# Optimization experiments

Measured on AMD Instinct MI355X. Metric: run time of the kernel, lower is better.

The kernel has to match this reference:

```python
import jax, jax.numpy as jnp
import numpy as np

B, H, W = 8, 160, 180
PHASES = 3
DELTA = 0.01
GAMMA = 1.0


def _conv(a, k):
    return jax.lax.conv_general_dilated(a, k, (1, 1), 'SAME',
                                        dimension_numbers=('NCHW', 'OIHW', 'NCHW'))


def _cconv(xr, xi, kr, ki):
    # complex conv via 4 real convs: (xr+i xi) * (kr+i ki)
    return _conv(xr, kr) - _conv(xi, ki), _conv(xr, ki) + _conv(xi, kr)


def _t(k):
    # conv_transpose2d(stride=1, pad=1, 3x3) == conv2d with swapped in/out channels and spatially flipped kernel
    return jnp.flip(jnp.swapaxes(k, 0, 1), axis=(2, 3))


def _cconvT(xr, xi, kr, ki):
    return _cconv(xr, xi, _t(kr), _t(ki))


def _act(x):
    # eq. (33): smoothed ReLU; quadratic inside |x| <= delta
    return jnp.where(jnp.abs(x) > DELTA, jax.nn.relu(x),
                     x * x / (4 * DELTA) + 0.5 * x + DELTA / 4)


def _act_der(x):
    return jnp.where(jnp.abs(x) > DELTA, (x > 0).astype(x.dtype),
                     x / (2 * DELTA) + 0.5)


def _grad_r(xc, convs, thr):
    # gradient of smoothed L2-channel-norm regularizer (grad_r_x1 / grad_r_x2)
    xr = jnp.real(xc).reshape(-1, 1, H, W)
    xi = jnp.imag(xc).reshape(-1, 1, H, W)
    acts = []
    ar, ai = xr, xi
    for kr, ki in convs[:3]:
        pr, pi = _cconv(ar, ai, kr, ki)
        ar, ai = _act(pr), _act(pi)
        acts.append((ar, ai))
    w4r, w4i = _cconv(ar, ai, *convs[3])
    norm = jnp.sqrt(jnp.sum(w4r * w4r + w4i * w4i, axis=1, keepdims=True))
    I1 = (norm > thr).astype(w4r.dtype)
    denom = jnp.maximum(norm, 1e-12)  # F.normalize eps
    gr = I1 * (w4r / denom) + (1 - I1) * (w4r / thr)
    gi = I1 * (w4i / denom) + (1 - I1) * (w4i / thr)
    gr, gi = _cconvT(gr, gi, *convs[3])
    for j in (2, 1, 0):
        # NOTE: faithful to source — derivative evaluated at the ACTIVATED values, complex multiply
        dr, di = _act_der(acts[j][0]), _act_der(acts[j][1])
        gr, gi = gr * dr - gi * di, gr * di + gi * dr
        gr, gi = _cconvT(gr, gi, *convs[j])
    return (gr + 1j * gi).reshape(-1, H, W)


def _grad_f(xc, kc, mask):
    # F^H( M o (M o F x - k) ): mriAdjointOp(mriForwardOp(x,m) - k, m)
    return jnp.fft.ifft2((jnp.fft.fft2(xc) * mask - kc) * mask)


def _forward(x1, x2, k1, k2, mask, convsA, convsB, thr1, thr2, a1, a2, b1, b2):
    to_c = lambda a: a[:, 0] + 1j * a[:, 1]
    x1c, x2c, k1c, k2c = to_c(x1), to_c(x2), to_c(k1), to_c(k2)
    for i in range(PHASES):
        x1c = x1c - a1[i] * _grad_f(x1c, k1c, mask) - b1[i] * _grad_r(x1c, convsA, thr1[0] * GAMMA)
        x2c = x2c - a2[i] * _grad_f(x2c, k2c, mask) - b2[i] * _grad_r(x2c, convsB, thr2[0] * GAMMA)
    return jnp.stack([jnp.real(x1c), jnp.imag(x1c), jnp.real(x2c), jnp.imag(x2c)], axis=1)


def setup_inputs() -> dict:
    key = jax.random.key(0)
    ks = jax.random.split(key, 32)
    d = {}
    d['x1'] = jax.random.normal(ks[0], (B, 2, H, W), jnp.float32)
    d['x2'] = jax.random.normal(ks[1], (B, 2, H, W), jnp.float32)
    d['k1'] = jax.random.normal(ks[2], (B, 2, H, W), jnp.float32)
    d['k2'] = jax.random.normal(ks[3], (B, 2, H, W), jnp.float32)
    d['mask'] = jax.random.uniform(ks[4], (H, W), jnp.float32)
    conv_names = ['conv1r', 'conv1i', 'conv2r', 'conv2i', 'conv3r', 'conv3i', 'conv4r', 'conv4i',
                  'conv1r_', 'conv1i_', 'conv2r_', 'conv2i_', 'conv3r_', 'conv3i_', 'conv4r_', 'conv4i_']
    for j, name in enumerate(conv_names):
        cin = 1 if name.startswith('conv1') else 32
        d[name] = 0.06 * jax.random.normal(ks[5 + j], (32, cin, 3, 3), jnp.float32)  # ~xavier
    d['soft_thr1'] = jnp.full((1,), 0.01, jnp.float32)
    d['soft_thr2'] = jnp.full((1,), 0.01, jnp.float32)
    d['alphas1'] = jnp.full((PHASES,), 0.5, jnp.float32)
    d['alphas2'] = jnp.full((PHASES,), 0.5, jnp.float32)
    d['betas1'] = jnp.full((PHASES,), 0.1, jnp.float32)
    d['betas2'] = jnp.full((PHASES,), 0.1, jnp.float32)
    return d


def reference(x1, x2, k1, k2, mask,
              conv1r, conv1i, conv2r, conv2i, conv3r, conv3i, conv4r, conv4i,
              conv1r_, conv1i_, conv2r_, conv2i_, conv3r_, conv3i_, conv4r_, conv4i_,
              soft_thr1, soft_thr2, alphas1, alphas2, betas1, betas2):
    convsA = [(conv1r, conv1i), (conv2r, conv2i), (conv3r, conv3i), (conv4r, conv4i)]
    convsB = [(conv1r_, conv1i_), (conv2r_, conv2i_), (conv3r_, conv3i_), (conv4r_, conv4i_)]
    return _forward(x1, x2, k1, k2, mask, convsA, convsB,
                    soft_thr1, soft_thr2, alphas1, alphas2, betas1, betas2)
```

## Files before the change

kernel.cpp:

```cpp
#include <hip/hip_runtime.h>
#include <math.h>

#define HH 160
#define WW 180
#define HWSZ (HH*WW)
#define BB 8
#define BB2 16
#define P1 ((size_t)BB*HWSZ)
#define PE2 ((size_t)BB2*32*HWSZ)

typedef unsigned short u16;
typedef unsigned long long ull;
typedef __attribute__((ext_vector_type(8))) short short8;
typedef __attribute__((ext_vector_type(2))) unsigned long long ull2;
typedef __attribute__((ext_vector_type(4))) float floatx4;

struct Ptrs16 { const float* p[16]; };

__device__ __forceinline__ u16 f2b(float f) {
  unsigned u = __builtin_bit_cast(unsigned, f);
  unsigned r = (u + 0x7fffu + ((u >> 16) & 1u)) >> 16;
  return (u16)r;
}
__device__ __forceinline__ float b2f(u16 h) {
  return __builtin_bit_cast(float, ((unsigned)h) << 16);
}

__device__ __forceinline__ float actf(float x) {
  float q = x*x*25.0f + 0.5f*x + 0.0025f;
  float r = fmaxf(x, 0.0f);
  return (fabsf(x) > 0.01f) ? r : q;
}
__device__ __forceinline__ float actdf(float x) {
  float q = x*50.0f + 0.5f;
  float r = (x > 0.0f) ? 1.0f : 0.0f;
  return (fabsf(x) > 0.01f) ? r : q;
}

__global__ void prep_all(Ptrs16 ps, u16* __restrict__ dst0) {
  const int rIdx[12] = {2,4,6,6,4,2,10,12,14,14,12,10};
  const int bwdF[12] = {0,0,0,1,1,1,0,0,0,1,1,1};
  int slot = blockIdx.x / 36;
  int idx = (blockIdx.x % 36)*256 + threadIdx.x;
  if (idx >= 9*32*32) return;
  const float* wr = ps.p[rIdx[slot]];
  const float* wi = ps.p[rIdx[slot]+1];
  u16* dst = dst0 + (size_t)slot*18432;
  int tap = idx >> 10; int rem = idx & 1023; int o = rem >> 5; int c = rem & 31;
  int s = bwdF[slot] ? ((c*32 + o)*9 + (8 - tap)) : ((o*32 + c)*9 + tap);
  float vr = wr[s], vi = wi[s];
  int nt = o >> 4, m = o & 15;
  size_t base = (((size_t)tap*2 + nt)*2*16 + (size_t)m)*32 + c;
  dst[base]       = f2b(vr);
  dst[base + 512] = f2b(vi);
}

template<int MODE>
__global__ __launch_bounds__(256, 6)
void conv_mfma(const u16* __restrict__ inb, const u16* __restrict__ wbA,
               const u16* __restrict__ wbB, u16* __restrict__ outb,
               const u16* __restrict__ derb,
               const float* __restrict__ thrA, const float* __restrict__ thrB)
{
  __shared__ alignas(128) u16 stg[2*6*34*32];
  const int tid = threadIdx.x;
  const int lane = tid & 63, wv = tid >> 6;
  const int x0 = blockIdx.x * 32, y0 = blockIdx.y * 4, b = blockIdx.z;
  const u16* wb = (b < BB) ? wbA : wbB;
  const int m = lane & 15, q = lane >> 4;

  for (int j = tid; j < 1632; j += 256) {
    int prow = j / 136; int rem = j - prow*136;
    int col = rem >> 2, chq = rem & 3;
    int plane = prow / 6, row = prow - plane*6;
    int gy = y0 - 1 + row, gx = x0 - 1 + col;
    ull v0 = 0, v1 = 0;
    if (gy >= 0 && gy < HH && gx >= 0 && gx < WW) {
      const ull* src = (const ull*)(inb + (size_t)plane*PE2
                                    + (((size_t)b*HH + gy)*WW + gx)*32 + chq*8);
      v0 = src[0]; v1 = src[1];
    }
    int B = prow*2176 + col*64 + chq*16;
    B ^= ((B >> 7) & 7) << 4;
    ull* dst = (ull*)((char*)stg + B);
    dst[0] = v0; dst[1] = v1;
  }
  __syncthreads();

  floatx4 accr[2][2], acci[2][2];
#pragma unroll
  for (int s = 0; s < 2; ++s)
#pragma unroll
    for (int nt = 0; nt < 2; ++nt) {
      accr[s][nt] = (floatx4){0.f,0.f,0.f,0.f};
      acci[s][nt] = (floatx4){0.f,0.f,0.f,0.f};
    }

#pragma unroll
  for (int tap = 0; tap < 9; ++tap) {
    const int ky = tap / 3, kx = tap - ky*3;
    short8 Pr[2], Pi[2];
#pragma unroll
    for (int s = 0; s < 2; ++s) {
      int col = s*16 + m + kx;
      int BR = ((wv + ky)*34 + col)*64 + q*16;
      int BI = BR + 13056;
      BR ^= ((BR >> 7) & 7) << 4;
      BI ^= ((BI >> 7) & 7) << 4;
      const ull* pR = (const ull*)((const char*)stg + BR);
      const ull* pI = (const ull*)((const char*)stg + BI);
      ull2 vr; vr.x = pR[0]; vr.y = pR[1];
      ull2 vi; vi.x = pI[0]; vi.y = pI[1];
      Pr[s] = __builtin_bit_cast(short8, vr);
      Pi[s] = __builtin_bit_cast(short8, vi);
    }
#pragma unroll
    for (int nt = 0; nt < 2; ++nt) {
      const u16* pw = wb + (size_t)(tap*2 + nt)*1024 + (size_t)m*32 + q*8;
      short8 Wr = *(const short8*)pw;
      short8 Wi = *(const short8*)(pw + 512);
      ull2 wx = __builtin_bit_cast(ull2, Wi);
      wx.x ^= 0x8000800080008000ULL;
      wx.y ^= 0x8000800080008000ULL;
      short8 nWi = __builtin_bit_cast(short8, wx);
#pragma unroll
      for (int s = 0; s < 2; ++s) {
        accr[s][nt] = __builtin_amdgcn_mfma_f32_16x16x32_bf16(Wr,  Pr[s], accr[s][nt], 0, 0, 0);
        accr[s][nt] = __builtin_amdgcn_mfma_f32_16x16x32_bf16(nWi, Pi[s], accr[s][nt], 0, 0, 0);
        acci[s][nt] = __builtin_amdgcn_mfma_f32_16x16x32_bf16(Wr,  Pi[s], acci[s][nt], 0, 0, 0);
        acci[s][nt] = __builtin_amdgcn_mfma_f32_16x16x32_bf16(Wi,  Pr[s], acci[s][nt], 0, 0, 0);
      }
    }
  }

  const int y = y0 + wv;
#pragma unroll
  for (int s = 0; s < 2; ++s) {
    int x = x0 + s*16 + m;
    bool ok = (x < WW);
    float invn = 1.0f;
    if constexpr (MODE == 3) {
      float ss = 0.f;
#pragma unroll
      for (int nt = 0; nt < 2; ++nt)
#pragma unroll
        for (int r = 0; r < 4; ++r)
          ss += accr[s][nt][r]*accr[s][nt][r] + acci[s][nt][r]*acci[s][nt][r];
      ss += __shfl_xor(ss, 16, 64);
      ss += __shfl_xor(ss, 32, 64);
      float thr = (b < BB ? thrA : thrB)[0];
      invn = 1.0f / fmaxf(sqrtf(ss), thr);
    }
    size_t pxbase = (((size_t)b*HH + y)*WW + x)*32;
#pragma unroll
    for (int nt = 0; nt < 2; ++nt) {
      size_t gb = pxbase + nt*16 + q*4;
      ull dR = 0, dI = 0;
      if constexpr (MODE == 2) {
        if (ok) { dR = *(const ull*)(derb + gb); dI = *(const ull*)(derb + PE2 + gb); }
      }
      ull vR = 0, vI = 0;
#pragma unroll
      for (int r = 0; r < 4; ++r) {
        float pr = accr[s][nt][r], pi = acci[s][nt][r];
        if constexpr (MODE == 1) { pr = actf(pr); pi = actf(pi); }
        if constexpr (MODE == 3) { pr *= invn; pi *= invn; }
        if constexpr (MODE == 2) {
          float dr = actdf(b2f((u16)(dR >> (16*r))));
          float di = actdf(b2f((u16)(dI >> (16*r))));
          float nr = pr*dr - pi*di;
          pi = pr*di + pi*dr; pr = nr;
        }
        vR |= (ull)f2b(pr) << (16*r);
        vI |= (ull)f2b(pi) << (16*r);
      }
      if (ok) {
        *(ull*)(outb + gb)       = vR;
        *(ull*)(outb + PE2 + gb) = vI;
      }
    }
  }
}

__global__ __launch_bounds__(256)
void l1fwd(const float* __restrict__ xall,
           const float* __restrict__ wrA, const float* __restrict__ wiA,
           const float* __restrict__ wrB, const float* __restrict__ wiB,
           u16* __restrict__ outb)
{
  __shared__ float hR[10][12], hI[10][12];
  __shared__ float wt[9][32][2];
  const int tid = threadIdx.x;
  const int og = tid & 3, px = tid >> 2;
  const int lx = px & 7, ly = px >> 3;
  const int x0 = blockIdx.x*8, y0 = blockIdx.y*8, b = blockIdx.z;
  const int branch = b >> 3, img = b & 7;
  const float* wr = branch ? wrB : wrA;
  const float* wi = branch ? wiB : wiA;
  const float* xp = xall + (size_t)branch*2*P1 + (size_t)img*HWSZ;

  for (int j = tid; j < 576; j += 256) {
    int tap = j >> 6; int rem = j & 63; int o = rem >> 1, ri = rem & 1;
    wt[tap][o][ri] = ri ? wi[o*9+tap] : wr[o*9+tap];
  }
  for (int j = tid; j < 200; j += 256) {
    int plane = j / 100; int pos = j - plane*100;
    int yy = pos / 10, xx = pos - yy*10;
    int gy = y0 - 1 + yy, gx = x0 - 1 + xx;
    float v = 0.f;
    if (gy >= 0 && gy < HH && gx >= 0 && gx < WW)
      v = xp[(size_t)plane*P1 + (size_t)gy*WW + gx];
    (plane ? hI : hR)[yy][xx] = v;
  }
  __syncthreads();

  float accR[8], accI[8];
#pragma unroll
  for (int o = 0; o < 8; ++o) { accR[o] = 0.f; accI[o] = 0.f; }
#pragma unroll
  for (int tap = 0; tap < 9; ++tap) {
    int ky = tap/3, kx = tap - ky*3;
    float ar = hR[ly+ky][lx+kx], ai = hI[ly+ky][lx+kx];
#pragma unroll
    for (int o = 0; o < 8; ++o) {
      float wrv = wt[tap][og*8+o][0], wiv = wt[tap][og*8+o][1];
      accR[o] += ar*wrv - ai*wiv;
      accI[o] += ar*wiv + ai*wrv;
    }
  }
  int gx = x0 + lx, gy = y0 + ly;
  if (gx < WW) {
    size_t base = (((size_t)b*HH + gy)*WW + gx)*32 + og*8;
    ull* dR = (ull*)(outb + base);
    ull* dI = (ull*)(outb + PE2 + base);
#pragma unroll
    for (int k = 0; k < 2; ++k) {
      ull vR = 0, vI = 0;
#pragma unroll
      for (int t = 0; t < 4; ++t) {
        vR |= (ull)f2b(actf(accR[k*4+t])) << (16*t);
        vI |= (ull)f2b(actf(accI[k*4+t])) << (16*t);
      }
      dR[k] = vR; dI[k] = vI;
    }
  }
}

__global__ __launch_bounds__(256)
void l1bwd(const u16* __restrict__ gb,
           const float* __restrict__ wrA, const float* __restrict__ wiA,
           const float* __restrict__ wrB, const float* __restrict__ wiB,
           float* __restrict__ outp)
{
  __shared__ alignas(16) u16 stg[2*100*32];
  __shared__ float wt[32][9][2];
  const int tid = threadIdx.x;
  const int cg = tid & 3, px = tid >> 2;
  const int lx = px & 7, ly = px >> 3;
  const int x0 = blockIdx.x*8, y0 = blockIdx.y*8, b = blockIdx.z;
  const int branch = b >> 3, img = b & 7;
  const float* wr = branch ? wrB : wrA;
  const float* wi = branch ? wiB : wiA;

  for (int j = tid; j < 576; j += 256) {
    int c = j / 18; int rem = j - c*18; int tap = rem >> 1, ri = rem & 1;
    wt[c][tap][ri] = (ri ? wi : wr)[c*9 + (8-tap)];
  }
  for (int j = tid; j < 800; j += 256) {
    int plane = j / 400; int rem = j - plane*400;
    int pos = rem >> 2, chq = rem & 3;
    int yy = pos / 10, xx = pos - yy*10;
    int gy = y0 - 1 + yy, gx = x0 - 1 + xx;
    ull v0 = 0, v1 = 0;
    if (gy >= 0 && gy < HH && gx >= 0 && gx < WW) {
      const ull* src = (const ull*)(gb + (size_t)plane*PE2
                                    + (((size_t)b*HH + gy)*WW + gx)*32 + chq*8);
      v0 = src[0]; v1 = src[1];
    }
    ull* dst = (ull*)&stg[((size_t)plane*100 + pos)*32 + chq*8];
    dst[0] = v0; dst[1] = v1;
  }
  __syncthreads();

  float gr = 0.f, gi = 0.f;
#pragma unroll
  for (int tap = 0; tap < 9; ++tap) {
    int ky = tap/3, kx = tap - ky*3;
    int pos = (ly+ky)*10 + (lx+kx);
    const ull* pR = (const ull*)&stg[(size_t)pos*32 + cg*8];
    const ull* pI = (const ull*)&stg[(100 + (size_t)pos)*32 + cg*8];
    ull r0 = pR[0], r1 = pR[1], i0 = pI[0], i1 = pI[1];
#pragma unroll
    for (int t = 0; t < 4; ++t) {
      int c = cg*8 + t;
      float ar = b2f((u16)(r0 >> (16*t))), ai = b2f((u16)(i0 >> (16*t)));
      float wrv = wt[c][tap][0], wiv = wt[c][tap][1];
      gr += ar*wrv - ai*wiv;
      gi += ar*wiv + ai*wrv;
    }
#pragma unroll
    for (int t = 0; t < 4; ++t) {
      int c = cg*8 + 4 + t;
      float ar = b2f((u16)(r1 >> (16*t))), ai = b2f((u16)(i1 >> (16*t)));
      float wrv = wt[c][tap][0], wiv = wt[c][tap][1];
      gr += ar*wrv - ai*wiv;
      gi += ar*wiv + ai*wrv;
    }
  }
  gr += __shfl_xor(gr, 1, 64); gr += __shfl_xor(gr, 2, 64);
  gi += __shfl_xor(gi, 1, 64); gi += __shfl_xor(gi, 2, 64);

  int gx = x0 + lx, gy = y0 + ly;
  if (cg == 0 && gx < WW) {
    size_t o2 = (size_t)branch*2*P1 + (size_t)img*HWSZ + (size_t)gy*WW + gx;
    outp[o2]      = gr;
    outp[P1 + o2] = gi;
  }
}

__global__ void gen_dft2(float2* __restrict__ Mf, float2* __restrict__ Mi, int N) {
  int idx = blockIdx.x*256 + threadIdx.x;
  if (idx >= N*N) return;
  int r = idx / N, c = idx - r*N;
  long mm = ((long)r * (long)c) % N;
  double a = 2.0 * 3.14159265358979323846 * (double)mm / (double)N;
  double cs = cos(a), sn = sin(a);
  Mf[idx] = make_float2((float)cs, (float)(-sn));
  Mi[idx] = make_float2((float)(cs/N), (float)(sn/N));
}

__global__ void dft_row_planes(const float* __restrict__ xall,
                               float2* __restrict__ out, const float2* __restrict__ M) {
  int bh = blockIdx.x;
  int v = threadIdx.x; if (v >= WW) return;
  int b2 = bh / HH, h = bh - b2*HH;
  int branch = b2 >> 3, img = b2 & 7;
  const float* rowR = xall + (size_t)branch*2*P1 + (size_t)img*HWSZ + (size_t)h*WW;
  const float* rowI = rowR + P1;
  float ar = 0.f, ai = 0.f;
  for (int w = 0; w < WW; ++w) {
    float sr = rowR[w], si = rowI[w];
    float2 m = M[w*WW + v];
    ar += sr*m.x - si*m.y;
    ai += sr*m.y + si*m.x;
  }
  out[(size_t)bh*WW + v] = make_float2(ar, ai);
}

__global__ void dft_row_c(const float2* __restrict__ in, float2* __restrict__ out,
                          const float2* __restrict__ M) {
  int bh = blockIdx.x;
  int v = threadIdx.x; if (v >= WW) return;
  const float2* row = in + (size_t)bh*WW;
  float ar = 0.f, ai = 0.f;
  for (int w = 0; w < WW; ++w) {
    float2 s = row[w];
    float2 m = M[w*WW + v];
    ar += s.x*m.x - s.y*m.y;
    ai += s.x*m.y + s.y*m.x;
  }
  out[(size_t)bh*WW + v] = make_float2(ar, ai);
}

__global__ void dft_col_c(const float2* __restrict__ in, float2* __restrict__ out,
                          const float2* __restrict__ M) {
  int bu = blockIdx.x;
  int v = threadIdx.x; if (v >= WW) return;
  int b = bu / HH, u = bu - b*HH;
  const float2* base = in + (size_t)b*HWSZ;
  float ar = 0.f, ai = 0.f;
  for (int h = 0; h < HH; ++h) {
    float2 m = M[u*HH + h];
    float2 s = base[(size_t)h*WW + v];
    ar += s.x*m.x - s.y*m.y;
    ai += s.x*m.y + s.y*m.x;
  }
  out[(size_t)bu*WW + v] = make_float2(ar, ai);
}

__global__ void dft_col_mask(const float2* __restrict__ in, float2* __restrict__ out,
                             const float2* __restrict__ M, const float* __restrict__ mask) {
  int bu = blockIdx.x;
  int v = threadIdx.x; if (v >= WW) return;
  int b = bu / HH, u = bu - b*HH;
  const float2* base = in + (size_t)b*HWSZ;
  float ar = 0.f, ai = 0.f;
  for (int h = 0; h < HH; ++h) {
    float mk = mask[h*WW + v]; float mm = mk*mk;
    float2 m = M[u*HH + h];
    float2 s = base[(size_t)h*WW + v];
    float sr = s.x*mm, si = s.y*mm;
    ar += sr*m.x - si*m.y;
    ai += sr*m.y + si*m.x;
  }
  out[(size_t)bu*WW + v] = make_float2(ar, ai);
}

__global__ void dft_row_update(const float2* __restrict__ in, const float2* __restrict__ M,
                               const float2* __restrict__ ctall, const float* __restrict__ grp,
                               float* __restrict__ xall,
                               const float* __restrict__ al1, const float* __restrict__ al2,
                               const float* __restrict__ be1, const float* __restrict__ be2,
                               int phase) {
  int bh = blockIdx.x;
  int v = threadIdx.x; if (v >= WW) return;
  int b2 = bh / HH, h = bh - b2*HH;
  int branch = b2 >> 3, img = b2 & 7;
  const float2* row = in + (size_t)bh*WW;
  float ar = 0.f, ai = 0.f;
  for (int w = 0; w < WW; ++w) {
    float2 s = row[w];
    float2 m = M[w*WW + v];
    ar += s.x*m.x - s.y*m.y;
    ai += s.x*m.y + s.y*m.x;
  }
  float2 ct = ctall[(size_t)bh*WW + v];
  float a   = (branch ? al2 : al1)[phase];
  float bet = (branch ? be2 : be1)[phase];
  size_t xo = (size_t)branch*2*P1 + (size_t)img*HWSZ + (size_t)h*WW + v;
  xall[xo]      -= a*(ar - ct.x) + bet*grp[xo];
  xall[P1 + xo] -= a*(ai - ct.y) + bet*grp[P1 + xo];
}

__global__ void maskk_m(const float* __restrict__ k1, const float* __restrict__ k2,
                        const float* __restrict__ mask, float2* __restrict__ t) {
  int i = blockIdx.x*256 + threadIdx.x;
  if (i >= (int)(2*P1)) return;
  int branch = i >= (int)P1;
  int ii = i - branch*(int)P1;
  int b = ii / HWSZ, p = ii - b*HWSZ;
  const float* k = branch ? k2 : k1;
  float m = mask[p];
  t[i] = make_float2(m * k[(size_t)b*2*HWSZ + p], m * k[(size_t)b*2*HWSZ + HWSZ + p]);
}

__global__ void unpack_m(const float* __restrict__ x1, const float* __restrict__ x2,
                         float* __restrict__ xall) {
  int i = blockIdx.x*256 + threadIdx.x;
  if (i >= (int)(2*P1)) return;
  int branch = i >= (int)P1;
  int ii = i - branch*(int)P1;
  int b = ii / HWSZ, p = ii - b*HWSZ;
  const float* src = branch ? x2 : x1;
  size_t dst = (size_t)branch*2*P1 + (size_t)b*HWSZ + p;
  xall[dst]      = src[(size_t)b*2*HWSZ + p];
  xall[P1 + dst] = src[(size_t)b*2*HWSZ + HWSZ + p];
}

__global__ void pack_kernel(const float* __restrict__ xall, float* __restrict__ out) {
  int i = blockIdx.x*256 + threadIdx.x;
  if (i >= (int)P1) return;
  int b = i / HWSZ, p = i - b*HWSZ;
  size_t ob = (size_t)b*4*HWSZ;
  size_t x1o = (size_t)b*HWSZ + p;
  size_t x2o = 2*P1 + x1o;
  out[ob + p]          = xall[x1o];
  out[ob + HWSZ + p]   = xall[P1 + x1o];
  out[ob + 2*HWSZ + p] = xall[x2o];
  out[ob + 3*HWSZ + p] = xall[P1 + x2o];
}

extern "C" void kernel_launch(void* const* d_in, const int* in_sizes, int n_in,
                              void* d_out, int out_size, void* d_ws, size_t ws_size,
                              hipStream_t stream) {
  (void)in_sizes; (void)n_in; (void)out_size; (void)ws_size;
  const float* x1in = (const float*)d_in[0];
  const float* x2in = (const float*)d_in[1];
  const float* k1   = (const float*)d_in[2];
  const float* k2   = (const float*)d_in[3];
  const float* mask = (const float*)d_in[4];
  Ptrs16 cw;
  for (int i = 0; i < 16; ++i) cw.p[i] = (const float*)d_in[5+i];
  const float* thr1 = (const float*)d_in[21];
  const float* thr2 = (const float*)d_in[22];
  const float* al1  = (const float*)d_in[23];
  const float* al2  = (const float*)d_in[24];
  const float* be1  = (const float*)d_in[25];
  const float* be2  = (const float*)d_in[26];
  float* out = (float*)d_out;

  u16* U = (u16*)d_ws;
  size_t uoff = 0;
  auto alloc_u = [&](size_t n){ u16* p = U + uoff; uoff += (n + 15) & ~(size_t)15; return p; };
  u16* act1 = alloc_u(2*PE2);
  u16* act2 = alloc_u(2*PE2);
  u16* act3 = alloc_u(2*PE2);
  u16* w4b  = alloc_u(2*PE2);
  u16* wp0  = alloc_u(12*18432);

  float* F = (float*)(U + uoff);
  size_t off = 0;
  auto alloc_f = [&](size_t n){ float* p = F + off; off += (n + 3) & ~(size_t)3; return p; };
  float*  xall = alloc_f(4*P1);
  float*  grp  = alloc_f(4*P1);
  float2* t1   = (float2*)alloc_f(4*P1);
  float2* t2   = (float2*)alloc_f(4*P1);
  float2* ctall= (float2*)alloc_f(4*P1);
  float2* EWf  = (float2*)alloc_f(2*(size_t)WW*WW);
  float2* EWi  = (float2*)alloc_f(2*(size_t)WW*WW);
  float2* EHf  = (float2*)alloc_f(2*(size_t)HH*HH);
  float2* EHi  = (float2*)alloc_f(2*(size_t)HH*HH);

  const dim3 MG(6, 40, BB2);
  const dim3 LG(23, 20, BB2);
  const int NP1 = (int)((P1 + 255)/256);
  const int NP2 = (int)((2*P1 + 255)/256);
  const int DFTG = BB2*HH;
  const int DFTB = 192;

  gen_dft2<<<(WW*WW+255)/256, 256, 0, stream>>>(EWf, EWi, WW);
  gen_dft2<<<(HH*HH+255)/256, 256, 0, stream>>>(EHf, EHi, HH);
  prep_all<<<12*36, 256, 0, stream>>>(cw, wp0);
  unpack_m<<<NP2, 256, 0, stream>>>(x1in, x2in, xall);

  maskk_m<<<NP2, 256, 0, stream>>>(k1, k2, mask, t1);
  dft_col_c<<<DFTG, DFTB, 0, stream>>>(t1, t2, EHi);
  dft_row_c<<<DFTG, DFTB, 0, stream>>>(t2, ctall, EWi);

  u16* WA[6]; u16* WB[6];
  for (int i = 0; i < 6; ++i) { WA[i] = wp0 + (size_t)i*18432; WB[i] = wp0 + (size_t)(6+i)*18432; }

  for (int ph = 0; ph < 3; ++ph) {
    l1fwd<<<LG, 256, 0, stream>>>(xall, cw.p[0], cw.p[1], cw.p[8], cw.p[9], act1);
    conv_mfma<1><<<MG, 256, 0, stream>>>(act1, WA[0], WB[0], act2, nullptr, nullptr, nullptr);
    conv_mfma<1><<<MG, 256, 0, stream>>>(act2, WA[1], WB[1], act3, nullptr, nullptr, nullptr);
    conv_mfma<3><<<MG, 256, 0, stream>>>(act3, WA[2], WB[2], w4b, nullptr, thr1, thr2);
    conv_mfma<2><<<MG, 256, 0, stream>>>(w4b,  WA[3], WB[3], act3, act3, nullptr, nullptr);
    conv_mfma<2><<<MG, 256, 0, stream>>>(act3, WA[4], WB[4], act2, act2, nullptr, nullptr);
    conv_mfma<2><<<MG, 256, 0, stream>>>(act2, WA[5], WB[5], act1, act1, nullptr, nullptr);
    l1bwd<<<LG, 256, 0, stream>>>(act1, cw.p[0], cw.p[1], cw.p[8], cw.p[9], grp);
    dft_row_planes<<<DFTG, DFTB, 0, stream>>>(xall, t1, EWf);
    dft_col_c<<<DFTG, DFTB, 0, stream>>>(t1, t2, EHf);
    dft_col_mask<<<DFTG, DFTB, 0, stream>>>(t2, t1, EHi, mask);
    dft_row_update<<<DFTG, DFTB, 0, stream>>>(t1, EWi, ctall, grp, xall,
                                              al1, al2, be1, be2, ph);
  }

  pack_kernel<<<NP1, 256, 0, stream>>>(xall, out);
}
```

Baseline: 2.028 ms.

## Process 20 rows per conv block with register-prefetched ring-buffered halo rows

Each conv_mfma block now walks five 4-row sub-tiles (20 rows) instead of one. It keeps a 12-row ring buffer in LDS and prefetches the next 4 input rows into registers while the MFMAs of the current sub-tile run. This is meant to cut redundant halo loads and block launch overhead, and to overlap global loads with compute. In exchange the LDS use doubles, occupancy drops to 3 blocks, the grid shrinks to 8 row-blocks (fewer blocks to fill the GPU), and an extra __syncthreads is added per sub-tile.

```diff
diff --git a/kernel.cpp b/kernel.cpp
--- a/kernel.cpp
+++ b/kernel.cpp
@@ -56,129 +56,176 @@
 }
 
 template<int MODE>
-__global__ __launch_bounds__(256, 6)
+__global__ __launch_bounds__(256, 3)
 void conv_mfma(const u16* __restrict__ inb, const u16* __restrict__ wbA,
                const u16* __restrict__ wbB, u16* __restrict__ outb,
                const u16* __restrict__ derb,
                const float* __restrict__ thrA, const float* __restrict__ thrB)
 {
-  __shared__ alignas(128) u16 stg[2*6*34*32];
+  __shared__ alignas(128) u16 stg[2*12*34*32];
   const int tid = threadIdx.x;
   const int lane = tid & 63, wv = tid >> 6;
-  const int x0 = blockIdx.x * 32, y0 = blockIdx.y * 4, b = blockIdx.z;
+  const int x0 = blockIdx.x * 32, y0 = blockIdx.y * 20, b = blockIdx.z;
   const u16* wb = (b < BB) ? wbA : wbB;
   const int m = lane & 15, q = lane >> 4;
 
   for (int j = tid; j < 1632; j += 256) {
     int prow = j / 136; int rem = j - prow*136;
     int col = rem >> 2, chq = rem & 3;
-    int plane = prow / 6, row = prow - plane*6;
-    int gy = y0 - 1 + row, gx = x0 - 1 + col;
+    int plane = prow / 6, o = prow - plane*6;
+    int gy = y0 - 1 + o, gx = x0 - 1 + col;
     ull v0 = 0, v1 = 0;
     if (gy >= 0 && gy < HH && gx >= 0 && gx < WW) {
       const ull* src = (const ull*)(inb + (size_t)plane*PE2
                                     + (((size_t)b*HH + gy)*WW + gx)*32 + chq*8);
       v0 = src[0]; v1 = src[1];
     }
-    int B = prow*2176 + col*64 + chq*16;
+    int B = plane*26112 + (o*34 + col)*64 + chq*16;
     B ^= ((B >> 7) & 7) << 4;
     ull* dst = (ull*)((char*)stg + B);
     dst[0] = v0; dst[1] = v1;
   }
   __syncthreads();
 
-  floatx4 accr[2][2], acci[2][2];
-#pragma unroll
-  for (int s = 0; s < 2; ++s)
-#pragma unroll
-    for (int nt = 0; nt < 2; ++nt) {
-      accr[s][nt] = (floatx4){0.f,0.f,0.f,0.f};
-      acci[s][nt] = (floatx4){0.f,0.f,0.f,0.f};
-    }
-
-#pragma unroll
-  for (int tap = 0; tap < 9; ++tap) {
-    const int ky = tap / 3, kx = tap - ky*3;
-    short8 Pr[2], Pi[2];
+  for (int t = 0; t < 5; ++t) {
+    const int t4 = t*4;
+    const bool pref = (t < 4);
+
+    ull va0[5], va1[5];
+    if (pref) {
+#pragma unroll
+      for (int it = 0; it < 5; ++it) {
+        va0[it] = 0; va1[it] = 0;
+        int j = tid + it*256;
+        if (j < 1088) {
+          int prow = j / 136; int rem = j - prow*136;
+          int col = rem >> 2, chq = rem & 3;
+          int k = prow >> 1, plane = prow & 1;
+          int gy = y0 + t4 + 5 + k, gx = x0 - 1 + col;
+          if (gy < HH && gx >= 0 && gx < WW) {
+            const ull* src = (const ull*)(inb + (size_t)plane*PE2
+                                          + (((size_t)b*HH + gy)*WW + gx)*32 + chq*8);
+            va0[it] = src[0]; va1[it] = src[1];
+          }
+        }
+      }
+      __builtin_amdgcn_sched_barrier(0);
+    }
+
+    floatx4 accr[2][2], acci[2][2];
+#pragma unroll
+    for (int s = 0; s < 2; ++s)
+#pragma unroll
+      for (int nt = 0; nt < 2; ++nt) {
+        accr[s][nt] = (floatx4){0.f,0.f,0.f,0.f};
+        acci[s][nt] = (floatx4){0.f,0.f,0.f,0.f};
+      }
+
+#pragma unroll
+    for (int tap = 0; tap < 9; ++tap) {
+      const int ky = tap / 3, kx = tap - ky*3;
+      int ro = t4 + wv + ky;
+      int slot = (ro >= 12) ? ro - 12 : ro;
+      short8 Pr[2], Pi[2];
+#pragma unroll
+      for (int s = 0; s < 2; ++s) {
+        int col = s*16 + m + kx;
+        int BR = (slot*34 + col)*64 + q*16;
+        int BI = BR + 26112;
+        BR ^= ((BR >> 7) & 7) << 4;
+        BI ^= ((BI >> 7) & 7) << 4;
+        const ull* pR = (const ull*)((const char*)stg + BR);
+        const ull* pI = (const ull*)((const char*)stg + BI);
+        ull2 vr; vr.x = pR[0]; vr.y = pR[1];
+        ull2 vi; vi.x = pI[0]; vi.y = pI[1];
+        Pr[s] = __builtin_bit_cast(short8, vr);
+        Pi[s] = __builtin_bit_cast(short8, vi);
+      }
+#pragma unroll
+      for (int nt = 0; nt < 2; ++nt) {
+        const u16* pw = wb + (size_t)(tap*2 + nt)*1024 + (size_t)m*32 + q*8;
+        short8 Wr = *(const short8*)pw;
+        short8 Wi = *(const short8*)(pw + 512);
+        ull2 wx = __builtin_bit_cast(ull2, Wi);
+        wx.x ^= 0x8000800080008000ULL;
+        wx.y ^= 0x8000800080008000ULL;
+        short8 nWi = __builtin_bit_cast(short8, wx);
+#pragma unroll
+        for (int s = 0; s < 2; ++s) {
+          accr[s][nt] = __builtin_amdgcn_mfma_f32_16x16x32_bf16(Wr,  Pr[s], accr[s][nt], 0, 0, 0);
+          accr[s][nt] = __builtin_amdgcn_mfma_f32_16x16x32_bf16(nWi, Pi[s], accr[s][nt], 0, 0, 0);
+          acci[s][nt] = __builtin_amdgcn_mfma_f32_16x16x32_bf16(Wr,  Pi[s], acci[s][nt], 0, 0, 0);
+          acci[s][nt] = __builtin_amdgcn_mfma_f32_16x16x32_bf16(Wi,  Pr[s], acci[s][nt], 0, 0, 0);
+        }
+      }
+    }
+
+    if (pref) {
+#pragma unroll
+      for (int it = 0; it < 5; ++it) {
+        int j = tid + it*256;
+        if (j < 1088) {
+          int prow = j / 136; int rem = j - prow*136;
+          int col = rem >> 2, chq = rem & 3;
+          int k = prow >> 1, plane = prow & 1;
+          int s = t4 + 6 + k; if (s >= 12) s -= 12;
+          int B = plane*26112 + (s*34 + col)*64 + chq*16;
+          B ^= ((B >> 7) & 7) << 4;
+          ull* dst = (ull*)((char*)stg + B);
+          dst[0] = va0[it]; dst[1] = va1[it];
+        }
+      }
+    }
+
+    const int y = y0 + t4 + wv;
 #pragma unroll
     for (int s = 0; s < 2; ++s) {
-      int col = s*16 + m + kx;
-      int BR = ((wv + ky)*34 + col)*64 + q*16;
-      int BI = BR + 13056;
-      BR ^= ((BR >> 7) & 7) << 4;
-      BI ^= ((BI >> 7) & 7) << 4;
-      const ull* pR = (const ull*)((const char*)stg + BR);
-      const ull* pI = (const ull*)((const char*)stg + BI);
-      ull2 vr; vr.x = pR[0]; vr.y = pR[1];
-      ull2 vi; vi.x = pI[0]; vi.y = pI[1];
-      Pr[s] = __builtin_bit_cast(short8, vr);
-      Pi[s] = __builtin_bit_cast(short8, vi);
-    }
-#pragma unroll
-    for (int nt = 0; nt < 2; ++nt) {
-      const u16* pw = wb + (size_t)(tap*2 + nt)*1024 + (size_t)m*32 + q*8;
-      short8 Wr = *(const short8*)pw;
-      short8 Wi = *(const short8*)(pw + 512);
-      ull2 wx = __builtin_bit_cast(ull2, Wi);
-      wx.x ^= 0x8000800080008000ULL;
-      wx.y ^= 0x8000800080008000ULL;
-      short8 nWi = __builtin_bit_cast(short8, wx);
-#pragma unroll
-      for (int s = 0; s < 2; ++s) {
-        accr[s][nt] = __builtin_amdgcn_mfma_f32_16x16x32_bf16(Wr,  Pr[s], accr[s][nt], 0, 0, 0);
-        accr[s][nt] = __builtin_amdgcn_mfma_f32_16x16x32_bf16(nWi, Pi[s], accr[s][nt], 0, 0, 0);
-        acci[s][nt] = __builtin_amdgcn_mfma_f32_16x16x32_bf16(Wr,  Pi[s], acci[s][nt], 0, 0, 0);
-        acci[s][nt] = __builtin_amdgcn_mfma_f32_16x16x32_bf16(Wi,  Pr[s], acci[s][nt], 0, 0, 0);
-      }
-    }
-  }
-
-  const int y = y0 + wv;
-#pragma unroll
-  for (int s = 0; s < 2; ++s) {
-    int x = x0 + s*16 + m;
-    bool ok = (x < WW);
-    float invn = 1.0f;
-    if constexpr (MODE == 3) {
-      float ss = 0.f;
-#pragma unroll
-      for (int nt = 0; nt < 2; ++nt)
-#pragma unroll
-        for (int r = 0; r < 4; ++r)
-          ss += accr[s][nt][r]*accr[s][nt][r] + acci[s][nt][r]*acci[s][nt][r];
-      ss += __shfl_xor(ss, 16, 64);
-      ss += __shfl_xor(ss, 32, 64);
-      float thr = (b < BB ? thrA : thrB)[0];
-      invn = 1.0f / fmaxf(sqrtf(ss), thr);
-    }
-    size_t pxbase = (((size_t)b*HH + y)*WW + x)*32;
-#pragma unroll
-    for (int nt = 0; nt < 2; ++nt) {
-      size_t gb = pxbase + nt*16 + q*4;
-      ull dR = 0, dI = 0;
-      if constexpr (MODE == 2) {
-        if (ok) { dR = *(const ull*)(derb + gb); dI = *(const ull*)(derb + PE2 + gb); }
-      }
-      ull vR = 0, vI = 0;
-#pragma unroll
-      for (int r = 0; r < 4; ++r) {
-        float pr = accr[s][nt][r], pi = acci[s][nt][r];
-        if constexpr (MODE == 1) { pr = actf(pr); pi = actf(pi); }
-        if constexpr (MODE == 3) { pr *= invn; pi *= invn; }
+      int x = x0 + s*16 + m;
+      bool ok = (x < WW);
+      float invn = 1.0f;
+      if constexpr (MODE == 3) {
+        float ss = 0.f;
+#pragma unroll
+        for (int nt = 0; nt < 2; ++nt)
+#pragma unroll
+          for (int r = 0; r < 4; ++r)
+            ss += accr[s][nt][r]*accr[s][nt][r] + acci[s][nt][r]*acci[s][nt][r];
+        ss += __shfl_xor(ss, 16, 64);
+        ss += __shfl_xor(ss, 32, 64);
+        float thr = (b < BB ? thrA : thrB)[0];
+        invn = 1.0f / fmaxf(sqrtf(ss), thr);
+      }
+      size_t pxbase = (((size_t)b*HH + y)*WW + x)*32;
+#pragma unroll
+      for (int nt = 0; nt < 2; ++nt) {
+        size_t gb = pxbase + nt*16 + q*4;
+        ull dR = 0, dI = 0;
         if constexpr (MODE == 2) {
-          float dr = actdf(b2f((u16)(dR >> (16*r))));
-          float di = actdf(b2f((u16)(dI >> (16*r))));
-          float nr = pr*dr - pi*di;
-          pi = pr*di + pi*dr; pr = nr;
+          if (ok) { dR = *(const ull*)(derb + gb); dI = *(const ull*)(derb + PE2 + gb); }
         }
-        vR |= (ull)f2b(pr) << (16*r);
-        vI |= (ull)f2b(pi) << (16*r);
-      }
-      if (ok) {
-        *(ull*)(outb + gb)       = vR;
-        *(ull*)(outb + PE2 + gb) = vI;
-      }
-    }
+        ull vR = 0, vI = 0;
+#pragma unroll
+        for (int r = 0; r < 4; ++r) {
+          float pr = accr[s][nt][r], pi = acci[s][nt][r];
+          if constexpr (MODE == 1) { pr = actf(pr); pi = actf(pi); }
+          if constexpr (MODE == 3) { pr *= invn; pi *= invn; }
+          if constexpr (MODE == 2) {
+            float dr = actdf(b2f((u16)(dR >> (16*r))));
+            float di = actdf(b2f((u16)(dI >> (16*r))));
+            float nr = pr*dr - pi*di;
+            pi = pr*di + pi*dr; pr = nr;
+          }
+          vR |= (ull)f2b(pr) << (16*r);
+          vI |= (ull)f2b(pi) << (16*r);
+        }
+        if (ok) {
+          *(ull*)(outb + gb)       = vR;
+          *(ull*)(outb + PE2 + gb) = vI;
+        }
+      }
+    }
+
+    __syncthreads();
   }
 }
 
@@ -501,7 +548,7 @@
   float2* EHf  = (float2*)alloc_f(2*(size_t)HH*HH);
   float2* EHi  = (float2*)alloc_f(2*(size_t)HH*HH);
 
-  const dim3 MG(6, 40, BB2);
+  const dim3 MG(6, 8, BB2);
   const dim3 LG(23, 20, BB2);
   const int NP1 = (int)((P1 + 255)/256);
   const int NP2 = (int)((2*P1 + 255)/256);
```

Measured after the change: 4.030 ms. 1.99x slower.

## Fuse conv4 forward, normalization and transposed conv4 into one halo-recompute kernel

Applied to the files above, without the earlier changes.

Adds a conv_f34 kernel that stages a 2-pixel halo tile of act3 in shared memory and computes the conv4 forward plus channel-norm scaling on a 6x34 halo region. It writes the scaled result back into shared memory and then applies the transposed conv4 and the activation-derivative multiply in the same block. This replaces two launches and removes the w4b global round trip. The cost is redundant halo computation (204 positions vs 128 outputs per block), extra syncthreads, larger shared memory use that may lower occupancy, and MODE 3 being removed from conv_mfma.

```diff
diff --git a/kernel.cpp b/kernel.cpp
--- a/kernel.cpp
+++ b/kernel.cpp
@@ -138,19 +138,6 @@
   for (int s = 0; s < 2; ++s) {
     int x = x0 + s*16 + m;
     bool ok = (x < WW);
-    float invn = 1.0f;
-    if constexpr (MODE == 3) {
-      float ss = 0.f;
-#pragma unroll
-      for (int nt = 0; nt < 2; ++nt)
-#pragma unroll
-        for (int r = 0; r < 4; ++r)
-          ss += accr[s][nt][r]*accr[s][nt][r] + acci[s][nt][r]*acci[s][nt][r];
-      ss += __shfl_xor(ss, 16, 64);
-      ss += __shfl_xor(ss, 32, 64);
-      float thr = (b < BB ? thrA : thrB)[0];
-      invn = 1.0f / fmaxf(sqrtf(ss), thr);
-    }
     size_t pxbase = (((size_t)b*HH + y)*WW + x)*32;
 #pragma unroll
     for (int nt = 0; nt < 2; ++nt) {
@@ -164,13 +151,226 @@
       for (int r = 0; r < 4; ++r) {
         float pr = accr[s][nt][r], pi = acci[s][nt][r];
         if constexpr (MODE == 1) { pr = actf(pr); pi = actf(pi); }
-        if constexpr (MODE == 3) { pr *= invn; pi *= invn; }
         if constexpr (MODE == 2) {
           float dr = actdf(b2f((u16)(dR >> (16*r))));
           float di = actdf(b2f((u16)(dI >> (16*r))));
           float nr = pr*dr - pi*di;
           pi = pr*di + pi*dr; pr = nr;
         }
+        vR |= (ull)f2b(pr) << (16*r);
+        vI |= (ull)f2b(pi) << (16*r);
+      }
+      if (ok) {
+        *(ull*)(outb + gb)       = vR;
+        *(ull*)(outb + PE2 + gb) = vI;
+      }
+    }
+  }
+  (void)thrA; (void)thrB;
+}
+
+__global__ __launch_bounds__(256, 3)
+void conv_f34(const u16* __restrict__ inb,
+              const u16* __restrict__ wfA, const u16* __restrict__ wfB,
+              const u16* __restrict__ wbA, const u16* __restrict__ wbB,
+              u16* __restrict__ outb,
+              const float* __restrict__ thrA, const float* __restrict__ thrB)
+{
+  __shared__ alignas(128) u16 stg[18432];
+  const int tid = threadIdx.x;
+  const int lane = tid & 63, wv = tid >> 6;
+  const int x0 = blockIdx.x*32, y0 = blockIdx.y*4, b = blockIdx.z;
+  const u16* wf = (b < BB) ? wfA : wfB;
+  const u16* wbk = (b < BB) ? wbA : wbB;
+  const float thr = (b < BB ? thrA : thrB)[0];
+  const int m = lane & 15, q = lane >> 4;
+
+  for (int j = tid; j < 2304; j += 256) {
+    int prow = j / 144; int rem = j - prow*144;
+    int col = rem >> 2, chq = rem & 3;
+    int plane = prow >> 3, row = prow & 7;
+    int gy = y0 - 2 + row, gx = x0 - 2 + col;
+    ull v0 = 0, v1 = 0;
+    if (gy >= 0 && gy < HH && gx >= 0 && gx < WW) {
+      const ull* src = (const ull*)(inb + (size_t)plane*PE2
+                                    + (((size_t)b*HH + gy)*WW + gx)*32 + chq*8);
+      v0 = src[0]; v1 = src[1];
+    }
+    int B = (prow*36 + col)*64 + chq*16;
+    B ^= ((B >> 7) & 7) << 4;
+    ull* dst = (ull*)((char*)stg + B);
+    dst[0] = v0; dst[1] = v1;
+  }
+  __syncthreads();
+
+  ull exR[2][2], exI[2][2];
+#pragma unroll
+  for (int s = 0; s < 2; ++s)
+#pragma unroll
+    for (int nt = 0; nt < 2; ++nt) {
+      int BA = ((2 + wv)*36 + (2 + s*16 + m))*64 + nt*32 + q*8;
+      int BI = BA + 18432;
+      BA ^= ((BA >> 7) & 7) << 4;
+      BI ^= ((BI >> 7) & 7) << 4;
+      exR[s][nt] = *(const ull*)((const char*)stg + BA);
+      exI[s][nt] = *(const ull*)((const char*)stg + BI);
+    }
+
+  const int ng = (wv == 3) ? 4 : 3;
+  ull pRk[4][2], pIk[4][2];
+#pragma unroll
+  for (int gi = 0; gi < 4; ++gi) {
+    if (gi < ng) {
+      int g = wv*3 + gi;
+      int p = g*16 + m;
+      bool pv = (p < 204);
+      int irow = pv ? (p / 34) : 0;
+      int icol = pv ? (p - irow*34) : 0;
+      floatx4 fr[2], fi[2];
+#pragma unroll
+      for (int nt = 0; nt < 2; ++nt) {
+        fr[nt] = (floatx4){0.f,0.f,0.f,0.f};
+        fi[nt] = (floatx4){0.f,0.f,0.f,0.f};
+      }
+#pragma unroll
+      for (int tap = 0; tap < 9; ++tap) {
+        int ky = tap/3, kx = tap - ky*3;
+        int BA = ((irow + ky)*36 + (icol + kx))*64 + q*16;
+        int BI = BA + 18432;
+        BA ^= ((BA >> 7) & 7) << 4;
+        BI ^= ((BI >> 7) & 7) << 4;
+        const ull* pR = (const ull*)((const char*)stg + BA);
+        const ull* pI = (const ull*)((const char*)stg + BI);
+        ull2 vr; vr.x = pR[0]; vr.y = pR[1];
+        ull2 vi; vi.x = pI[0]; vi.y = pI[1];
+        short8 Pr = __builtin_bit_cast(short8, vr);
+        short8 Pi = __builtin_bit_cast(short8, vi);
+#pragma unroll
+        for (int nt = 0; nt < 2; ++nt) {
+          const u16* pw = wf + (size_t)(tap*2 + nt)*1024 + (size_t)m*32 + q*8;
+          short8 Wr = *(const short8*)pw;
+          short8 Wi = *(const short8*)(pw + 512);
+          ull2 wx = __builtin_bit_cast(ull2, Wi);
+          wx.x ^= 0x8000800080008000ULL;
+          wx.y ^= 0x8000800080008000ULL;
+          short8 nWi = __builtin_bit_cast(short8, wx);
+          fr[nt] = __builtin_amdgcn_mfma_f32_16x16x32_bf16(Wr,  Pr, fr[nt], 0, 0, 0);
+          fr[nt] = __builtin_amdgcn_mfma_f32_16x16x32_bf16(nWi, Pi, fr[nt], 0, 0, 0);
+          fi[nt] = __builtin_amdgcn_mfma_f32_16x16x32_bf16(Wr,  Pi, fi[nt], 0, 0, 0);
+          fi[nt] = __builtin_amdgcn_mfma_f32_16x16x32_bf16(Wi,  Pr, fi[nt], 0, 0, 0);
+        }
+      }
+      float ss = 0.f;
+#pragma unroll
+      for (int nt = 0; nt < 2; ++nt)
+#pragma unroll
+        for (int r = 0; r < 4; ++r)
+          ss += fr[nt][r]*fr[nt][r] + fi[nt][r]*fi[nt][r];
+      ss += __shfl_xor(ss, 16, 64);
+      ss += __shfl_xor(ss, 32, 64);
+      float invn = 1.0f / fmaxf(sqrtf(ss), thr);
+      int gyi = y0 - 1 + irow, gxi = x0 - 1 + icol;
+      if (gyi < 0 || gyi >= HH || gxi < 0 || gxi >= WW) invn = 0.0f;
+#pragma unroll
+      for (int nt = 0; nt < 2; ++nt) {
+        ull vR = 0, vI = 0;
+#pragma unroll
+        for (int r = 0; r < 4; ++r) {
+          vR |= (ull)f2b(fr[nt][r]*invn) << (16*r);
+          vI |= (ull)f2b(fi[nt][r]*invn) << (16*r);
+        }
+        pRk[gi][nt] = vR; pIk[gi][nt] = vI;
+      }
+    }
+  }
+  __syncthreads();
+
+#pragma unroll
+  for (int gi = 0; gi < 4; ++gi) {
+    if (gi < ng) {
+      int g = wv*3 + gi;
+      int p = g*16 + m;
+      if (p < 204) {
+        int irow = p / 34, icol = p - irow*34;
+        int base = (irow*34 + icol)*64;
+#pragma unroll
+        for (int nt = 0; nt < 2; ++nt) {
+          int BA = base + nt*32 + q*8;
+          int BI = BA + 13056;
+          BA ^= ((BA >> 7) & 7) << 4;
+          BI ^= ((BI >> 7) & 7) << 4;
+          *(ull*)((char*)stg + BA) = pRk[gi][nt];
+          *(ull*)((char*)stg + BI) = pIk[gi][nt];
+        }
+      }
+    }
+  }
+  __syncthreads();
+
+  floatx4 accr[2][2], acci[2][2];
+#pragma unroll
+  for (int s = 0; s < 2; ++s)
+#pragma unroll
+    for (int nt = 0; nt < 2; ++nt) {
+      accr[s][nt] = (floatx4){0.f,0.f,0.f,0.f};
+      acci[s][nt] = (floatx4){0.f,0.f,0.f,0.f};
+    }
+
+#pragma unroll
+  for (int tap = 0; tap < 9; ++tap) {
+    const int ky = tap / 3, kx = tap - ky*3;
+    short8 Pr[2], Pi[2];
+#pragma unroll
+    for (int s = 0; s < 2; ++s) {
+      int col = s*16 + m + kx;
+      int BR = ((wv + ky)*34 + col)*64 + q*16;
+      int BI = BR + 13056;
+      BR ^= ((BR >> 7) & 7) << 4;
+      BI ^= ((BI >> 7) & 7) << 4;
+      const ull* pR = (const ull*)((const char*)stg + BR);
+      const ull* pI = (const ull*)((const char*)stg + BI);
+      ull2 vr; vr.x = pR[0]; vr.y = pR[1];
+      ull2 vi; vi.x = pI[0]; vi.y = pI[1];
+      Pr[s] = __builtin_bit_cast(short8, vr);
+      Pi[s] = __builtin_bit_cast(short8, vi);
+    }
+#pragma unroll
+    for (int nt = 0; nt < 2; ++nt) {
+      const u16* pw = wbk + (size_t)(tap*2 + nt)*1024 + (size_t)m*32 + q*8;
+      short8 Wr = *(const short8*)pw;
+      short8 Wi = *(const short8*)(pw + 512);
+      ull2 wx = __builtin_bit_cast(ull2, Wi);
+      wx.x ^= 0x8000800080008000ULL;
+      wx.y ^= 0x8000800080008000ULL;
+      short8 nWi = __builtin_bit_cast(short8, wx);
+#pragma unroll
+      for (int s = 0; s < 2; ++s) {
+        accr[s][nt] = __builtin_amdgcn_mfma_f32_16x16x32_bf16(Wr,  Pr[s], accr[s][nt], 0, 0, 0);
+        accr[s][nt] = __builtin_amdgcn_mfma_f32_16x16x32_bf16(nWi, Pi[s], accr[s][nt], 0, 0, 0);
+        acci[s][nt] = __builtin_amdgcn_mfma_f32_16x16x32_bf16(Wr,  Pi[s], acci[s][nt], 0, 0, 0);
+        acci[s][nt] = __builtin_amdgcn_mfma_f32_16x16x32_bf16(Wi,  Pr[s], acci[s][nt], 0, 0, 0);
+      }
+    }
+  }
+
+  const int y = y0 + wv;
+#pragma unroll
+  for (int s = 0; s < 2; ++s) {
+    int x = x0 + s*16 + m;
+    bool ok = (x < WW);
+    size_t pxbase = (((size_t)b*HH + y)*WW + x)*32;
+#pragma unroll
+    for (int nt = 0; nt < 2; ++nt) {
+      size_t gb = pxbase + nt*16 + q*4;
+      ull dR = exR[s][nt], dI = exI[s][nt];
+      ull vR = 0, vI = 0;
+#pragma unroll
+      for (int r = 0; r < 4; ++r) {
+        float pr = accr[s][nt][r], pi = acci[s][nt][r];
+        float dr = actdf(b2f((u16)(dR >> (16*r))));
+        float di = actdf(b2f((u16)(dI >> (16*r))));
+        float nr = pr*dr - pi*di;
+        pi = pr*di + pi*dr; pr = nr;
         vR |= (ull)f2b(pr) << (16*r);
         vI |= (ull)f2b(pi) << (16*r);
       }
@@ -524,9 +724,8 @@
     l1fwd<<<LG, 256, 0, stream>>>(xall, cw.p[0], cw.p[1], cw.p[8], cw.p[9], act1);
     conv_mfma<1><<<MG, 256, 0, stream>>>(act1, WA[0], WB[0], act2, nullptr, nullptr, nullptr);
     conv_mfma<1><<<MG, 256, 0, stream>>>(act2, WA[1], WB[1], act3, nullptr, nullptr, nullptr);
-    conv_mfma<3><<<MG, 256, 0, stream>>>(act3, WA[2], WB[2], w4b, nullptr, thr1, thr2);
-    conv_mfma<2><<<MG, 256, 0, stream>>>(w4b,  WA[3], WB[3], act3, act3, nullptr, nullptr);
-    conv_mfma<2><<<MG, 256, 0, stream>>>(act3, WA[4], WB[4], act2, act2, nullptr, nullptr);
+    conv_f34<<<MG, 256, 0, stream>>>(act3, WA[2], WB[2], WA[3], WB[3], w4b, thr1, thr2);
+    conv_mfma<2><<<MG, 256, 0, stream>>>(w4b,  WA[4], WB[4], act2, act2, nullptr, nullptr);
     conv_mfma<2><<<MG, 256, 0, stream>>>(act2, WA[5], WB[5], act1, act1, nullptr, nullptr);
     l1bwd<<<LG, 256, 0, stream>>>(act1, cw.p[0], cw.p[1], cw.p[8], cw.p[9], grp);
     dft_row_planes<<<DFTG, DFTB, 0, stream>>>(xall, t1, EWf);
```

New measurement: 3.035 ms. 1.5x slower.
